# Kernel tuning notes

Measured on AMD Instinct MI355X. Metric: run time of the kernel, lower is better.

## Reference

```python
import jax, jax.numpy as jnp
import numpy as np
from jax import lax

T, B, F = 512, 256, 258
IN, H = 256, 1024


def setup_inputs() -> dict:
    key = jax.random.key(0)
    ks = jax.random.split(key, 6)

    def lin_w(k, fi, fo):
        return jax.random.normal(k, (fi, fo), jnp.float32) * (1.0 / np.sqrt(fi))

    return {
        "u": jax.random.normal(ks[0], (T, B, F), jnp.float32),
        "a": jnp.float32(0.92),
        "b": jnp.float32(-0.3),
        "W0": lin_w(ks[1], IN, H), "b0": jnp.zeros((H,), jnp.float32),
        "W1": lin_w(ks[2], H, H), "b1": jnp.zeros((H,), jnp.float32),
        "W2": lin_w(ks[3], H, H), "b2": jnp.zeros((H,), jnp.float32),
        "W3": lin_w(ks[4], H, 1), "b3": jnp.zeros((1,), jnp.float32),
    }


def reference(u, a, b, W0, b0, W1, b1, W2, b2, W3, b3):
    Tn, Bn, Fn = u.shape
    # MLP over cols 2: — independent of the recurrent state, so batch all timesteps.
    feats = u[:, :, 2:].reshape(Tn * Bn, Fn - 2)
    h = jax.nn.relu(feats @ W0 + b0)
    h = jax.nn.relu(h @ W1 + b1)
    h = jax.nn.relu(h @ W2 + b2)
    net = (h @ W3 + b3).reshape(Tn, Bn)  # [T, B]

    c1 = u[:, :, 1]  # [T, B], multiplied by b each step
    y0 = u[0, :, 0]  # u_y[0]; also the col-0 value used at j=0

    def step(carry, xs):
        net_j, c1_j = xs
        y = a * carry + b * c1_j + net_j
        return y, y

    _, ys = lax.scan(step, y0, (net, c1))  # ys: [T, B] = u_y[1:]
    return jnp.concatenate([y0[None, :], ys], axis=0)  # [T+1, B]
```

## Files before the change

kernel.cpp:

```cpp
#include <hip/hip_runtime.h>
#include <hip/hip_fp16.h>

typedef _Float16 v8h __attribute__((ext_vector_type(8)));
typedef _Float16 v4h __attribute__((ext_vector_type(4)));
typedef float v4f __attribute__((ext_vector_type(4)));

#define T_DIM 512
#define B_DIM 256
#define F_DIM 258
#define IN_DIM 256
#define H_DIM 1024
#define M_ROWS (T_DIM * B_DIM)

__device__ __forceinline__ void tile_map(int b, int nM, int nN, int& mt, int& nt) {
    if ((nM & 7) == 0) {
        int xcd = b & 7;
        int l = b >> 3;
        int mpx = nM >> 3;
        int lm = l / nN;
        mt = xcd * mpx + lm;
        nt = l - lm * nN;
    } else {
        int lm = b / nN;
        mt = lm;
        nt = b - lm * nN;
    }
}

__device__ __forceinline__ void gl16(const _Float16* g, _Float16* l) {
    __builtin_amdgcn_global_load_lds(
        (const __attribute__((address_space(1))) unsigned int*)g,
        (__attribute__((address_space(3))) unsigned int*)l, 16, 0, 0);
}


__global__ void prep_x_kernel(const float* __restrict__ u,
                              _Float16* __restrict__ X, int nrows) {
    int i = blockIdx.x * blockDim.x + threadIdx.x;
    int total = nrows * 32;
    int stride = gridDim.x * blockDim.x;
    for (; i < total; i += stride) {
        int r = ((i >> 9) << 4) + (i & 15);
        int kb = (i >> 4) & 31;
        const float* s = u + (size_t)r * 258 + 2 + kb * 8;
        _Float16 h[8];
#pragma unroll
        for (int j = 0; j < 8; ++j) h[j] = (_Float16)s[j];
        *(v8h*)(X + ((size_t)(r >> 4) * 32 + kb) * 128 + (r & 15) * 8) =
            *(v8h*)h;
    }
}

__global__ void prep_c1_kernel(const float* __restrict__ u,
                               float* __restrict__ c1, int nrows) {
    int r = blockIdx.x * blockDim.x + threadIdx.x;
    if (r < nrows) c1[r] = u[(size_t)r * 258 + 1];
}

__global__ void wt_frag_kernel(const float* __restrict__ W,
                               _Float16* __restrict__ BF, int K, int N) {
    int idx = blockIdx.x * blockDim.x + threadIdx.x;
    int total = (N >> 6) * (K >> 5) * 4 * 64;
    if (idx >= total) return;
    int l = idx & 63;
    int f = idx >> 6;
    int i = f & 3;
    int gk = f >> 2;
    int KC = K >> 5;
    int g = gk / KC, kc = gk - g * KC;
    int col = g * 64 + i * 16 + (l & 15);
    int krow = kc * 32 + (l >> 4) * 8;
    _Float16 tmp[8];
#pragma unroll
    for (int j = 0; j < 8; ++j) tmp[j] = (_Float16)W[(size_t)(krow + j) * N + col];
    *(v8h*)&BF[(size_t)idx * 8] = *(v8h*)tmp;
}

__global__ void wt_vec_kernel(const float* __restrict__ W,
                              _Float16* __restrict__ Wh, int K) {
    int i = blockIdx.x * blockDim.x + threadIdx.x;
    if (i < K) Wh[i] = (_Float16)W[i];
}

__global__ void zero_kernel(float* __restrict__ p, int n) {
    int i = blockIdx.x * blockDim.x + threadIdx.x;
    if (i < n) p[i] = 0.f;
}

template <int DOT>
__global__ __launch_bounds__(256, 4)
void gemm128(const _Float16* __restrict__ Xb, const _Float16* __restrict__ WF,
             const float* __restrict__ bias, const _Float16* __restrict__ w3,
             _Float16* __restrict__ Cb, float* __restrict__ net,
             int M, int N, int K) {
    extern __shared__ _Float16 lds[];
    const int tid = threadIdx.x;
    const int lane = tid & 63;
    const int wave = tid >> 6;
    const int wm = wave >> 1;
    const int wn = wave & 1;
    const int quad = lane >> 4;
    const int r16 = lane & 15;
    const int wm4 = wm * 4;
    const int lrb = lane * 8;

    int mt, nt;
    tile_map(blockIdx.x, M >> 7, N >> 7, mt, nt);
    const int m0 = mt * 128;
    const int n0 = nt * 128;

    const int KC = K >> 5;
    const int KC8 = K >> 3;
    const int NT = KC;
    const int m016 = m0 >> 4;
    const int nt2 = nt * 2;

    auto stageA = [&](int g, int kt, _Float16* pa) {
        gl16(WF + ((size_t)(nt2 + g) * KC + kt) * 2048 + tid * 8,
             pa + g * 2048 + tid * 8);
    };
    auto stageB = [&](int mb, int kt, _Float16* pb) {
        gl16(Xb + ((size_t)(m016 + mb + (tid >> 6)) * KC8 + (size_t)kt * 4) * 128 +
                 (tid & 63) * 8,
             pb + mb * 512 + tid * 8);
    };

    v4f acc[4][4];
#pragma unroll
    for (int i = 0; i < 4; ++i)
#pragma unroll
        for (int j = 0; j < 4; ++j) acc[i][j] = (v4f)0.f;

    {
        _Float16* A0 = lds;
        _Float16* B0 = lds + 4096;
        stageA(0, 0, A0); stageA(1, 0, A0);
        stageB(0, 0, B0); stageB(4, 0, B0);
        asm volatile("s_waitcnt vmcnt(0)" ::: "memory");
        __builtin_amdgcn_s_barrier();
    }

#pragma unroll 2
    for (int kt = 0; kt < NT; ++kt) {
        _Float16* pAc = lds + (kt & 1) * 8192;
        _Float16* pBc = pAc + 4096;
        _Float16* pAn = lds + ((kt + 1) & 1) * 8192;
        _Float16* pBn = pAn + 4096;
        const bool pre = (kt + 1 < NT);
        const int kn = kt + 1;

        v8h af[4], bf[4];
#pragma unroll
        for (int i = 0; i < 4; ++i)
            af[i] = *(const v8h*)(pAc + wn * 2048 + i * 512 + lrb);
#pragma unroll
        for (int mi = 0; mi < 4; ++mi)
            bf[mi] = *(const v8h*)(pBc + (wm4 + mi) * 512 + lrb);

        if (pre) {
            stageA(0, kn, pAn); stageA(1, kn, pAn);
            stageB(0, kn, pBn); stageB(4, kn, pBn);
        }

        __builtin_amdgcn_s_setprio(1);
#pragma unroll
        for (int mi = 0; mi < 4; ++mi)
#pragma unroll
            for (int ni = 0; ni < 4; ++ni)
                acc[mi][ni] = __builtin_amdgcn_mfma_f32_16x16x32_f16(
                    af[ni], bf[mi], acc[mi][ni], 0, 0, 0);
        __builtin_amdgcn_s_setprio(0);

        if (kt != NT - 1) {
            asm volatile("s_waitcnt vmcnt(0)" ::: "memory");
            __builtin_amdgcn_s_barrier();
        }
    }

    const int nb = n0 + wn * 64;
    v4f bv[4];
#pragma unroll
    for (int ni = 0; ni < 4; ++ni)
        bv[ni] = *(const v4f*)&bias[nb + ni * 16 + quad * 4];

    if constexpr (DOT == 0) {
        const int NC8 = N >> 3;
#pragma unroll
        for (int ni = 0; ni < 4; ++ni) {
            const int nblk = ((nb + ni * 16) >> 3) + (quad >> 1);
#pragma unroll
            for (int mi = 0; mi < 4; ++mi) {
                v4h hv;
#pragma unroll
                for (int i = 0; i < 4; ++i)
                    hv[i] = (_Float16)fmaxf(acc[mi][ni][i] + bv[ni][i], 0.f);
                const size_t mblk = (size_t)((m0 + wm * 64 + mi * 16) >> 4);
                _Float16* dst =
                    Cb + (mblk * NC8 + nblk) * 128 + r16 * 8 + (quad & 1) * 4;
                *(v4h*)dst = hv;
            }
        }
    } else {
        v4h wv[4];
#pragma unroll
        for (int ni = 0; ni < 4; ++ni)
            wv[ni] = *(const v4h*)&w3[nb + ni * 16 + quad * 4];
#pragma unroll
        for (int mi = 0; mi < 4; ++mi) {
            float t = 0.f;
#pragma unroll
            for (int ni = 0; ni < 4; ++ni)
#pragma unroll
                for (int i = 0; i < 4; ++i) {
                    float v = fmaxf(acc[mi][ni][i] + bv[ni][i], 0.f);
                    t = fmaf(v, (float)wv[ni][i], t);
                }
            t += __shfl_xor(t, 16);
            t += __shfl_xor(t, 32);
            if (quad == 0) {
                int row = m0 + wm * 64 + mi * 16 + r16;
                atomicAdd(&net[row], t);
            }
        }
    }
}

__global__ void scan_kernel(const float* __restrict__ net,
                            const float* __restrict__ c1,
                            const float* __restrict__ u,
                            const float* __restrict__ pa,
                            const float* __restrict__ pb,
                            const float* __restrict__ pb3,
                            float* __restrict__ out) {
    const int bidx = threadIdx.x;
    const float a = pa[0];
    const float b = pb[0];
    const float b3 = pb3[0];
    float y = u[(size_t)bidx * F_DIM];
    out[bidx] = y;
#pragma unroll 8
    for (int t = 0; t < T_DIM; ++t) {
        float z = fmaf(b, c1[t * B_DIM + bidx], net[t * B_DIM + bidx] + b3);
        y = fmaf(a, y, z);
        out[(t + 1) * B_DIM + bidx] = y;
    }
}

extern "C" void kernel_launch(void* const* d_in, const int* in_sizes, int n_in,
                              void* d_out, int out_size, void* d_ws, size_t ws_size,
                              hipStream_t stream) {
    const float* u = (const float*)d_in[0];
    const float* pa = (const float*)d_in[1];
    const float* pb = (const float*)d_in[2];
    const float* W0 = (const float*)d_in[3];
    const float* b0 = (const float*)d_in[4];
    const float* W1 = (const float*)d_in[5];
    const float* b1 = (const float*)d_in[6];
    const float* W2 = (const float*)d_in[7];
    const float* b2 = (const float*)d_in[8];
    const float* W3 = (const float*)d_in[9];
    const float* b3 = (const float*)d_in[10];
    float* out = (float*)d_out;

    char* ws = (char*)d_ws;
    size_t off = 0;
    auto alloc = [&](size_t bytes) -> void* {
        void* p = ws + off;
        off += (bytes + 255) & ~(size_t)255;
        return p;
    };

    float* net = (float*)alloc((size_t)M_ROWS * 4);
    float* c1 = (float*)alloc((size_t)M_ROWS * 4);
    _Float16* W0F = (_Float16*)alloc((size_t)IN_DIM * H_DIM * 2);
    _Float16* W1F = (_Float16*)alloc((size_t)H_DIM * H_DIM * 2);
    _Float16* W2F = (_Float16*)alloc((size_t)H_DIM * H_DIM * 2);
    _Float16* W3h = (_Float16*)alloc((size_t)H_DIM * 2);

    const size_t per_row = 512 + 2048 + 2048;
    size_t avail = (ws_size > off + 65536) ? (ws_size - off - 65536) : 0;
    long Rl = (long)(avail / per_row);
    Rl = (Rl / 2048) * 2048;
    if (Rl < 2048) Rl = 2048;
    if (Rl > M_ROWS) Rl = M_ROWS;
    const int R = (int)Rl;

    _Float16* Xc = (_Float16*)alloc((size_t)R * IN_DIM * 2);
    _Float16* HAc = (_Float16*)alloc((size_t)R * H_DIM * 2);
    _Float16* HBc = (_Float16*)alloc((size_t)R * H_DIM * 2);

    wt_frag_kernel<<<(IN_DIM / 32) * (H_DIM / 64), 256, 0, stream>>>(W0, W0F,
                                                                     IN_DIM, H_DIM);
    wt_frag_kernel<<<(H_DIM / 32) * (H_DIM / 64), 256, 0, stream>>>(W1, W1F,
                                                                    H_DIM, H_DIM);
    wt_frag_kernel<<<(H_DIM / 32) * (H_DIM / 64), 256, 0, stream>>>(W2, W2F,
                                                                    H_DIM, H_DIM);
    wt_vec_kernel<<<4, 256, 0, stream>>>(W3, W3h, H_DIM);
    zero_kernel<<<M_ROWS / 256, 256, 0, stream>>>(net, M_ROWS);

    const size_t lds_bytes = 32768;
    for (int r0 = 0; r0 < M_ROWS; r0 += R) {
        int Mc = M_ROWS - r0;
        if (Mc > R) Mc = R;

        int pgrid = (Mc * 32 + 255) / 256;
        if (pgrid > 2048) pgrid = 2048;
        prep_x_kernel<<<pgrid, 256, 0, stream>>>(u + (size_t)r0 * F_DIM, Xc, Mc);
        prep_c1_kernel<<<(Mc + 255) / 256, 256, 0, stream>>>(
            u + (size_t)r0 * F_DIM, c1 + r0, Mc);

        dim3 blk(256);
        dim3 grd((Mc / 128) * (H_DIM / 128));
        gemm128<0><<<grd, blk, lds_bytes, stream>>>(Xc, W0F, b0, nullptr, HAc,
                                                    nullptr, Mc, H_DIM, IN_DIM);
        gemm128<0><<<grd, blk, lds_bytes, stream>>>(HAc, W1F, b1, nullptr, HBc,
                                                    nullptr, Mc, H_DIM, H_DIM);
        gemm128<1><<<grd, blk, lds_bytes, stream>>>(HBc, W2F, b2, W3h, nullptr,
                                                    net + r0, Mc, H_DIM, H_DIM);
    }

    scan_kernel<<<1, 256, 0, stream>>>(net, c1, u, pa, pb, b3, out);
}
```

Before: 939.8 us.

## Replace 128x128 GEMM with persistent 256x256-tile kernel and triple-buffered pipeline

Swaps the per-tile 128x128 GEMM for a persistent 512-thread kernel that computes 256x256 output tiles and loops over tiles with a grid-stride. It uses a three-stage LDS ring (96 KB), register double-buffering of fragments, and prefetches the next tile's first k-slices during the current tile's epilogue. The aims are more data reuse per tile, hidden global-load latency, and less launch and tail overhead. In exchange it uses more LDS and registers per block, which lowers occupancy, and the cross-tile prefetch and wait accounting is more complex.

```diff
diff --git a/kernel.cpp b/kernel.cpp
--- a/kernel.cpp
+++ b/kernel.cpp
@@ -88,139 +88,187 @@
 }
 
 template <int DOT>
-__global__ __launch_bounds__(256, 4)
-void gemm128(const _Float16* __restrict__ Xb, const _Float16* __restrict__ WF,
-             const float* __restrict__ bias, const _Float16* __restrict__ w3,
-             _Float16* __restrict__ Cb, float* __restrict__ net,
-             int M, int N, int K) {
+__global__ __launch_bounds__(512, 2)
+void gemm_pers(const _Float16* __restrict__ Xb, const _Float16* __restrict__ WF,
+               const float* __restrict__ bias, const _Float16* __restrict__ w3,
+               _Float16* __restrict__ Cb, float* __restrict__ net,
+               int M, int N, int K) {
     extern __shared__ _Float16 lds[];
     const int tid = threadIdx.x;
     const int lane = tid & 63;
     const int wave = tid >> 6;
-    const int wm = wave >> 1;
-    const int wn = wave & 1;
+    const int wm = wave >> 2;
+    const int wn = wave & 3;
     const int quad = lane >> 4;
     const int r16 = lane & 15;
-    const int wm4 = wm * 4;
+    const int wm8 = wm * 8;
     const int lrb = lane * 8;
 
-    int mt, nt;
-    tile_map(blockIdx.x, M >> 7, N >> 7, mt, nt);
-    const int m0 = mt * 128;
-    const int n0 = nt * 128;
-
+    const int nM = M >> 8, nN = N >> 8;
+    const int nOT = nM * nN;
     const int KC = K >> 5;
     const int KC8 = K >> 3;
-    const int NT = KC;
-    const int m016 = m0 >> 4;
-    const int nt2 = nt * 2;
-
-    auto stageA = [&](int g, int kt, _Float16* pa) {
-        gl16(WF + ((size_t)(nt2 + g) * KC + kt) * 2048 + tid * 8,
-             pa + g * 2048 + tid * 8);
+    const int NTk = KC;
+    const int gstride = gridDim.x;
+
+    auto stage = [&](int m016x, int nt4x, int ktx, _Float16* buf) {
+#pragma unroll
+        for (int op = 0; op < 2; ++op)
+            gl16(WF + ((size_t)(nt4x + op * 2 + (tid >> 8)) * KC + ktx) * 2048 +
+                     (tid & 255) * 8,
+                 buf + op * 4096 + tid * 8);
+#pragma unroll
+        for (int op = 0; op < 2; ++op)
+            gl16(Xb + ((size_t)(m016x + op * 8 + (tid >> 6)) * KC8 +
+                       (size_t)ktx * 4) * 128 + (tid & 63) * 8,
+                 buf + 8192 + op * 4096 + tid * 8);
     };
-    auto stageB = [&](int mb, int kt, _Float16* pb) {
-        gl16(Xb + ((size_t)(m016 + mb + (tid >> 6)) * KC8 + (size_t)kt * 4) * 128 +
-                 (tid & 63) * 8,
-             pb + mb * 512 + tid * 8);
-    };
-
-    v4f acc[4][4];
-#pragma unroll
-    for (int i = 0; i < 4; ++i)
+
+    v4f acc[8][4];
+#pragma unroll
+    for (int i = 0; i < 8; ++i)
 #pragma unroll
         for (int j = 0; j < 4; ++j) acc[i][j] = (v4f)0.f;
 
+    v8h afA[4], bfA[8], afB[4], bfB[8];
+    int bi = 0;
+
+    int oi = blockIdx.x;
+    if (oi >= nOT) return;
+
     {
-        _Float16* A0 = lds;
-        _Float16* B0 = lds + 4096;
-        stageA(0, 0, A0); stageA(1, 0, A0);
-        stageB(0, 0, B0); stageB(4, 0, B0);
-        asm volatile("s_waitcnt vmcnt(0)" ::: "memory");
+        int mt0, nt0;
+        tile_map(oi, nM, nN, mt0, nt0);
+        int m016p = mt0 * 16, nt4p = nt0 * 4;
+        stage(m016p, nt4p, 0, lds);
+        stage(m016p, nt4p, 1, lds + 16384);
+        stage(m016p, nt4p, 2, lds + 32768);
+        asm volatile("s_waitcnt vmcnt(4)" ::: "memory");
         __builtin_amdgcn_s_barrier();
-    }
-
-#pragma unroll 2
-    for (int kt = 0; kt < NT; ++kt) {
-        _Float16* pAc = lds + (kt & 1) * 8192;
-        _Float16* pBc = pAc + 4096;
-        _Float16* pAn = lds + ((kt + 1) & 1) * 8192;
-        _Float16* pBn = pAn + 4096;
-        const bool pre = (kt + 1 < NT);
-        const int kn = kt + 1;
-
-        v8h af[4], bf[4];
+        _Float16* pA = lds;
+        _Float16* pB = lds + 8192;
 #pragma unroll
         for (int i = 0; i < 4; ++i)
-            af[i] = *(const v8h*)(pAc + wn * 2048 + i * 512 + lrb);
-#pragma unroll
-        for (int mi = 0; mi < 4; ++mi)
-            bf[mi] = *(const v8h*)(pBc + (wm4 + mi) * 512 + lrb);
-
-        if (pre) {
-            stageA(0, kn, pAn); stageA(1, kn, pAn);
-            stageB(0, kn, pBn); stageB(4, kn, pBn);
+            afA[i] = *(const v8h*)(pA + wn * 2048 + i * 512 + lrb);
+#pragma unroll
+        for (int mi = 0; mi < 8; ++mi)
+            bfA[mi] = *(const v8h*)(pB + (wm8 + mi) * 512 + lrb);
+        asm volatile("s_waitcnt lgkmcnt(0)" ::: "memory");
+        __builtin_amdgcn_s_barrier();
+    }
+
+    for (; oi < nOT; oi += gstride) {
+        int mt, nt;
+        tile_map(oi, nM, nN, mt, nt);
+        const int m016 = mt * 16, nt4 = nt * 4;
+        const int m0 = mt * 256;
+        const int nb = nt * 256 + wn * 64;
+        const int oin = oi + gstride;
+        const bool has_next = (oin < nOT);
+        int m016n = 0, nt4n = 0;
+        if (has_next) {
+            int mtn, ntn;
+            tile_map(oin, nM, nN, mtn, ntn);
+            m016n = mtn * 16;
+            nt4n = ntn * 4;
         }
 
-        __builtin_amdgcn_s_setprio(1);
-#pragma unroll
-        for (int mi = 0; mi < 4; ++mi)
-#pragma unroll
-            for (int ni = 0; ni < 4; ++ni)
-                acc[mi][ni] = __builtin_amdgcn_mfma_f32_16x16x32_f16(
-                    af[ni], bf[mi], acc[mi][ni], 0, 0, 0);
-        __builtin_amdgcn_s_setprio(0);
-
-        if (kt != NT - 1) {
-            asm volatile("s_waitcnt vmcnt(0)" ::: "memory");
-            __builtin_amdgcn_s_barrier();
-        }
-    }
-
-    const int nb = n0 + wn * 64;
-    v4f bv[4];
-#pragma unroll
-    for (int ni = 0; ni < 4; ++ni)
-        bv[ni] = *(const v4f*)&bias[nb + ni * 16 + quad * 4];
-
-    if constexpr (DOT == 0) {
-        const int NC8 = N >> 3;
-#pragma unroll
-        for (int ni = 0; ni < 4; ++ni) {
-            const int nblk = ((nb + ni * 16) >> 3) + (quad >> 1);
-#pragma unroll
-            for (int mi = 0; mi < 4; ++mi) {
-                v4h hv;
+        auto step = [&](int k, v8h (&caf)[4], v8h (&cbf)[8], v8h (&naf)[4],
+                        v8h (&nbf)[8]) {
+            int bi1 = bi + 1;
+            if (bi1 == 3) bi1 = 0;
+            const bool ep = (k == NTk - 1);
+            if (!(ep && !has_next)) {
+                _Float16* pA = lds + bi1 * 16384;
+                _Float16* pB = pA + 8192;
 #pragma unroll
                 for (int i = 0; i < 4; ++i)
-                    hv[i] = (_Float16)fmaxf(acc[mi][ni][i] + bv[ni][i], 0.f);
-                const size_t mblk = (size_t)((m0 + wm * 64 + mi * 16) >> 4);
-                _Float16* dst =
-                    Cb + (mblk * NC8 + nblk) * 128 + r16 * 8 + (quad & 1) * 4;
-                *(v4h*)dst = hv;
+                    naf[i] = *(const v8h*)(pA + wn * 2048 + i * 512 + lrb);
+#pragma unroll
+                for (int mi = 0; mi < 8; ++mi)
+                    nbf[mi] = *(const v8h*)(pB + (wm8 + mi) * 512 + lrb);
             }
-        }
-    } else {
-        v4h wv[4];
-#pragma unroll
-        for (int ni = 0; ni < 4; ++ni)
-            wv[ni] = *(const v4h*)&w3[nb + ni * 16 + quad * 4];
-#pragma unroll
-        for (int mi = 0; mi < 4; ++mi) {
-            float t = 0.f;
-#pragma unroll
-            for (int ni = 0; ni < 4; ++ni)
-#pragma unroll
-                for (int i = 0; i < 4; ++i) {
-                    float v = fmaxf(acc[mi][ni][i] + bv[ni][i], 0.f);
-                    t = fmaf(v, (float)wv[ni][i], t);
+            __builtin_amdgcn_s_setprio(1);
+#pragma unroll
+            for (int mi = 0; mi < 8; ++mi)
+#pragma unroll
+                for (int ni = 0; ni < 4; ++ni)
+                    acc[mi][ni] = __builtin_amdgcn_mfma_f32_16x16x32_f16(
+                        caf[ni], cbf[mi], acc[mi][ni], 0, 0, 0);
+            __builtin_amdgcn_s_setprio(0);
+            if (ep) {
+                v4f bv[4];
+#pragma unroll
+                for (int ni = 0; ni < 4; ++ni)
+                    bv[ni] = *(const v4f*)&bias[nb + ni * 16 + quad * 4];
+                if constexpr (DOT == 0) {
+                    const int NC8 = N >> 3;
+#pragma unroll
+                    for (int ni = 0; ni < 4; ++ni) {
+                        const int nblk = ((nb + ni * 16) >> 3) + (quad >> 1);
+#pragma unroll
+                        for (int mi = 0; mi < 8; ++mi) {
+                            v4h hv;
+#pragma unroll
+                            for (int i = 0; i < 4; ++i)
+                                hv[i] = (_Float16)fmaxf(
+                                    acc[mi][ni][i] + bv[ni][i], 0.f);
+                            const size_t mblk =
+                                (size_t)((m0 + wm * 128 + mi * 16) >> 4);
+                            *(v4h*)(Cb + (mblk * NC8 + nblk) * 128 + r16 * 8 +
+                                    (quad & 1) * 4) = hv;
+                        }
+                    }
+                } else {
+                    v4h wv[4];
+#pragma unroll
+                    for (int ni = 0; ni < 4; ++ni)
+                        wv[ni] = *(const v4h*)&w3[nb + ni * 16 + quad * 4];
+#pragma unroll
+                    for (int mi = 0; mi < 8; ++mi) {
+                        float t = 0.f;
+#pragma unroll
+                        for (int ni = 0; ni < 4; ++ni)
+#pragma unroll
+                            for (int i = 0; i < 4; ++i) {
+                                float v =
+                                    fmaxf(acc[mi][ni][i] + bv[ni][i], 0.f);
+                                t = fmaf(v, (float)wv[ni][i], t);
+                            }
+                        t += __shfl_xor(t, 16);
+                        t += __shfl_xor(t, 32);
+                        if (quad == 0) {
+                            int row = m0 + wm * 128 + mi * 16 + r16;
+                            atomicAdd(&net[row], t);
+                        }
+                    }
                 }
-            t += __shfl_xor(t, 16);
-            t += __shfl_xor(t, 32);
-            if (quad == 0) {
-                int row = m0 + wm * 64 + mi * 16 + r16;
-                atomicAdd(&net[row], t);
+#pragma unroll
+                for (int i = 0; i < 8; ++i)
+#pragma unroll
+                    for (int j = 0; j < 4; ++j) acc[i][j] = (v4f)0.f;
             }
+            bool staged = true;
+            if (k + 3 < NTk)
+                stage(m016, nt4, k + 3, lds + bi * 16384);
+            else if (has_next)
+                stage(m016n, nt4n, k + 3 - NTk, lds + bi * 16384);
+            else
+                staged = false;
+            if (!(ep && !has_next)) {
+                if (staged)
+                    asm volatile("s_waitcnt vmcnt(4)" ::: "memory");
+                else
+                    asm volatile("s_waitcnt vmcnt(0)" ::: "memory");
+                asm volatile("s_waitcnt lgkmcnt(0)" ::: "memory");
+                __builtin_amdgcn_s_barrier();
+            }
+            bi = bi1;
+        };
+
+        for (int k = 0; k < NTk; k += 2) {
+            step(k, afA, bfA, afB, bfB);
+            step(k + 1, afB, bfB, afA, bfA);
         }
     }
 }
@@ -298,7 +346,7 @@
     wt_vec_kernel<<<4, 256, 0, stream>>>(W3, W3h, H_DIM);
     zero_kernel<<<M_ROWS / 256, 256, 0, stream>>>(net, M_ROWS);
 
-    const size_t lds_bytes = 32768;
+    const size_t lds_bytes = 98304;
     for (int r0 = 0; r0 < M_ROWS; r0 += R) {
         int Mc = M_ROWS - r0;
         if (Mc > R) Mc = R;
@@ -309,13 +357,14 @@
         prep_c1_kernel<<<(Mc + 255) / 256, 256, 0, stream>>>(
             u + (size_t)r0 * F_DIM, c1 + r0, Mc);
 
-        dim3 blk(256);
-        dim3 grd((Mc / 128) * (H_DIM / 128));
-        gemm128<0><<<grd, blk, lds_bytes, stream>>>(Xc, W0F, b0, nullptr, HAc,
+        int nOT = (Mc >> 8) * (H_DIM >> 8);
+        int g = nOT < 256 ? nOT : 256;
+        dim3 blk(512);
+        gemm_pers<0><<<g, blk, lds_bytes, stream>>>(Xc, W0F, b0, nullptr, HAc,
                                                     nullptr, Mc, H_DIM, IN_DIM);
-        gemm128<0><<<grd, blk, lds_bytes, stream>>>(HAc, W1F, b1, nullptr, HBc,
+        gemm_pers<0><<<g, blk, lds_bytes, stream>>>(HAc, W1F, b1, nullptr, HBc,
                                                     nullptr, Mc, H_DIM, H_DIM);
-        gemm128<1><<<grd, blk, lds_bytes, stream>>>(HBc, W2F, b2, W3h, nullptr,
+        gemm_pers<1><<<g, blk, lds_bytes, stream>>>(HBc, W2F, b2, W3h, nullptr,
                                                     net + r0, Mc, H_DIM, H_DIM);
     }
 
```

Result: slower. 1.727 ms (+83.8%).
